# Kernel optimization log

Measured on AMD Instinct MI355X. Metric: run time of the kernel, lower is better.

The kernel has to match this reference:

```python
import jax, jax.numpy as jnp
import numpy as np

B, S, HID = 2, 2048, 1024
H, D = 16, 64  # num query heads, head_dim; single shared KV head
SCALE = D ** -0.5


def setup_inputs() -> dict:
    key = jax.random.key(0)
    k1, k2, k3, k4, k5 = jax.random.split(key, 5)
    return {
        "hidden_states": jax.random.normal(k1, (B, S, HID), dtype=jnp.float32),
        "Wq": jax.random.normal(k2, (HID, HID), dtype=jnp.float32) * 0.02,
        "Wk": jax.random.normal(k3, (HID, D), dtype=jnp.float32) * 0.02,
        "Wv": jax.random.normal(k4, (HID, D), dtype=jnp.float32) * 0.02,
        "Wo": jax.random.normal(k5, (HID, HID), dtype=jnp.float32) * 0.02,
    }


def reference(hidden_states, Wq, Wk, Wv, Wo):
    b, s, _ = hidden_states.shape
    # projections: Q has H heads; K/V have a single shared head of dim D
    q = (hidden_states @ Wq).reshape(b, s, H, D)  # [B,S,H,D]
    k = hidden_states @ Wk                        # [B,S,D]
    v = hidden_states @ Wv                        # [B,S,D]
    # scores: broadcast single KV head across all query heads
    scores = jnp.einsum("bqhd,bkd->bhqk", q, k) * SCALE  # [B,H,S,S]
    attn = jax.nn.softmax(scores, axis=-1)
    out = jnp.einsum("bhqk,bkd->bqhd", attn, v).reshape(b, s, HID)
    return out @ Wo
```

## Files before the change

kernel.cpp:

```cpp
#include <hip/hip_runtime.h>
#include <math.h>

#define BATCH 2
#define SEQ   2048
#define HID   1024
#define NH    16
#define HD    64
#define MTOT  (BATCH * SEQ)

#define PST 72
#define WTS 69

#define EXP_C1 0.1803368801111255f
#define EXP_C2 (-17.312340490667562f)

typedef __attribute__((ext_vector_type(8))) short short8;
typedef __attribute__((ext_vector_type(4))) float floatx4;
typedef __attribute__((ext_vector_type(16))) float floatx16;
typedef __attribute__((ext_vector_type(4))) unsigned int uint4v;

#define MFMA32(a, b, c) __builtin_amdgcn_mfma_f32_32x32x16_bf16(a, b, c, 0, 0, 0)

static __device__ __forceinline__ floatx16 zero16() {
    floatx16 z;
    #pragma unroll
    for (int i = 0; i < 16; ++i) z[i] = 0.f;
    return z;
}

__device__ __forceinline__ unsigned short f2bf(float x) {
    unsigned u = __float_as_uint(x);
    u += 0x7FFF + ((u >> 16) & 1);
    return (unsigned short)(u >> 16);
}
__device__ __forceinline__ float bf2f(unsigned short h) {
    return __uint_as_float((unsigned)h << 16);
}
__device__ __forceinline__ void split16(const float* f, unsigned short* hh, unsigned short* ll) {
    #pragma unroll
    for (int e = 0; e < 16; ++e) {
        unsigned short h = f2bf(f[e]);
        hh[e] = h;
        ll[e] = f2bf(f[e] - bf2f(h));
    }
}

__global__ __launch_bounds__(256)
void presplit_kernel(const float* __restrict__ Wq, const float* __restrict__ Wk,
                     const float* __restrict__ Wv, const float* __restrict__ Wo,
                     const float* __restrict__ X,
                     unsigned short* __restrict__ WqTh, unsigned short* __restrict__ WqTl,
                     unsigned short* __restrict__ WkTh, unsigned short* __restrict__ WkTl,
                     unsigned short* __restrict__ WvTh, unsigned short* __restrict__ WvTl,
                     unsigned short* __restrict__ WoTh, unsigned short* __restrict__ WoTl,
                     unsigned short* __restrict__ Xh)
{
    __shared__ __align__(16) float Wtmp[64][WTS];
    const int tid = threadIdx.x;
    int bx = blockIdx.x;

    if (bx >= 544) {
        size_t i0 = (size_t)(bx - 544) * 4096 + tid * 16;
        float f[16];
        *(float4*)&f[0]  = *(const float4*)(X + i0 + 0);
        *(float4*)&f[4]  = *(const float4*)(X + i0 + 4);
        *(float4*)&f[8]  = *(const float4*)(X + i0 + 8);
        *(float4*)&f[12] = *(const float4*)(X + i0 + 12);
        unsigned short hh[16];
        #pragma unroll
        for (int e = 0; e < 16; ++e) hh[e] = f2bf(f[e]);
        *(uint4*)(Xh + i0)     = *(uint4*)&hh[0];
        *(uint4*)(Xh + i0 + 8) = *(uint4*)&hh[8];
        return;
    }

    const float* W; unsigned short *Th, *Tl; int ldw, kt, nt;
    if (bx < 256)      { W = Wq; Th = WqTh; Tl = WqTl; ldw = HID; kt = bx >> 4; nt = bx & 15; }
    else if (bx < 272) { W = Wk; Th = WkTh; Tl = WkTl; ldw = HD;  kt = bx - 256; nt = 0; }
    else if (bx < 288) { W = Wv; Th = WvTh; Tl = WvTl; ldw = HD;  kt = bx - 272; nt = 0; }
    else               { W = Wo; Th = WoTh; Tl = WoTl; ldw = HID; bx -= 288; kt = bx >> 4; nt = bx & 15; }
    const int k0 = kt * 64, n0 = nt * 64;

    {
        const int wk = tid >> 2, wn = (tid & 3) * 16;
        const float* wp = W + (size_t)(k0 + wk) * ldw + n0 + wn;
        float f[16];
        *(float4*)&f[0]  = *(const float4*)(wp + 0);
        *(float4*)&f[4]  = *(const float4*)(wp + 4);
        *(float4*)&f[8]  = *(const float4*)(wp + 8);
        *(float4*)&f[12] = *(const float4*)(wp + 12);
        #pragma unroll
        for (int e = 0; e < 16; ++e) Wtmp[wk][wn + e] = f[e];
    }
    __syncthreads();
    {
        const int rn = tid >> 2, rk = (tid & 3) * 16;
        float f[16];
        #pragma unroll
        for (int e = 0; e < 16; ++e) f[e] = Wtmp[rk + e][rn];
        unsigned short hh[16], ll[16];
        split16(f, hh, ll);
        size_t off = (size_t)(n0 + rn) * HID + k0 + rk;
        *(uint4*)(Th + off)     = *(uint4*)&hh[0];
        *(uint4*)(Th + off + 8) = *(uint4*)&hh[8];
        *(uint4*)(Tl + off)     = *(uint4*)&ll[0];
        *(uint4*)(Tl + off + 8) = *(uint4*)&ll[8];
    }
}

__global__ __launch_bounds__(256)
void qkv_kernel(const unsigned short* __restrict__ Xh,
                const unsigned short* __restrict__ WqTh, const unsigned short* __restrict__ WqTl,
                const unsigned short* __restrict__ WkTh, const unsigned short* __restrict__ WkTl,
                const unsigned short* __restrict__ WvTh, const unsigned short* __restrict__ WvTl,
                unsigned short* __restrict__ Qh,
                unsigned short* __restrict__ Kh, unsigned short* __restrict__ Vth)
{
    __shared__ __align__(16) unsigned short Ah[128][PST];
    __shared__ __align__(16) unsigned short Wsh[64][PST], Wsl[64][PST];

    const int tid  = threadIdx.x;
    const int wave = tid >> 6, lane = tid & 63;
    const int t = lane & 15, quad = lane >> 4;
    const int m0 = blockIdx.x * 128;
    const int nb = blockIdx.y;

    const unsigned short *WTh, *WTl; int n0b;
    if (nb < 16)       { WTh = WqTh; WTl = WqTl; n0b = nb * 64; }
    else if (nb == 16) { WTh = WkTh; WTl = WkTl; n0b = 0; }
    else               { WTh = WvTh; WTl = WvTl; n0b = 0; }

    floatx4 acc[2][4];
    #pragma unroll
    for (int mi = 0; mi < 2; ++mi)
        #pragma unroll
        for (int sub = 0; sub < 4; ++sub) acc[mi][sub] = (floatx4){0.f,0.f,0.f,0.f};

    for (int kt = 0; kt < HID / 64; ++kt) {
        __syncthreads();
        #pragma unroll
        for (int i = 0; i < 4; ++i) {
            int c = tid + i * 256;
            int row = c >> 3, col8 = (c & 7) * 8;
            *(uint4*)&Ah[row][col8] =
                *(const uint4*)(Xh + (size_t)(m0 + row) * HID + kt * 64 + col8);
        }
        #pragma unroll
        for (int i = 0; i < 2; ++i) {
            int c = tid + i * 256;
            int row = c >> 3, col8 = (c & 7) * 8;
            size_t g = (size_t)(n0b + row) * HID + kt * 64 + col8;
            *(uint4*)&Wsh[row][col8] = *(const uint4*)(WTh + g);
            *(uint4*)&Wsl[row][col8] = *(const uint4*)(WTl + g);
        }
        __syncthreads();
        #pragma unroll
        for (int ks = 0; ks < 2; ++ks) {
            short8 bh[4], bl[4];
            #pragma unroll
            for (int sub = 0; sub < 4; ++sub) {
                bh[sub] = *(const short8*)&Wsh[sub * 16 + t][ks * 32 + quad * 8];
                bl[sub] = *(const short8*)&Wsl[sub * 16 + t][ks * 32 + quad * 8];
            }
            #pragma unroll
            for (int mi = 0; mi < 2; ++mi) {
                short8 ah = *(const short8*)&Ah[wave * 32 + mi * 16 + t][ks * 32 + quad * 8];
                #pragma unroll
                for (int sub = 0; sub < 4; ++sub) {
                    acc[mi][sub] = __builtin_amdgcn_mfma_f32_16x16x32_bf16(ah, bh[sub], acc[mi][sub], 0, 0, 0);
                    acc[mi][sub] = __builtin_amdgcn_mfma_f32_16x16x32_bf16(ah, bl[sub], acc[mi][sub], 0, 0, 0);
                }
            }
        }
    }

    #pragma unroll
    for (int mi = 0; mi < 2; ++mi)
        #pragma unroll
        for (int sub = 0; sub < 4; ++sub)
            #pragma unroll
            for (int r = 0; r < 4; ++r) {
                int g = m0 + wave * 32 + mi * 16 + quad * 4 + r;
                int d = sub * 16 + t;
                unsigned short hh = f2bf(acc[mi][sub][r]);
                if (nb < 16) {
                    int b = g >> 11, s = g & (SEQ - 1);
                    Qh[((size_t)(b * NH + nb) * SEQ + s) * HD + d] = hh;
                } else if (nb == 16) {
                    Kh[(size_t)g * HD + d] = hh;
                } else {
                    int b = g >> 11, s = g & (SEQ - 1);
                    Vth[(size_t)b * HD * SEQ + (size_t)d * SEQ + s] = hh;
                }
            }
}

__global__ __launch_bounds__(512, 4)
void flash_kernel(const unsigned short* __restrict__ Qhg,
                  const unsigned short* __restrict__ Khg,
                  const unsigned short* __restrict__ Vthg,
                  unsigned short* __restrict__ Oh)
{
    __shared__ __align__(16) char smem[33792];
    unsigned short (*Ksh)[PST] = (unsigned short (*)[PST])smem;
    unsigned short (*Vsh)[PST] = (unsigned short (*)[PST])(smem + 64 * PST * 2);

    const int tid  = threadIdx.x;
    const int wave = tid >> 6, lane = tid & 63;
    const int lq = lane & 31, hi = lane >> 5;
    const int qw = wave >> 1;
    const int ks = wave & 1;

    const int q0 = blockIdx.x * 128;
    const int h  = blockIdx.y;
    const int b  = blockIdx.z;

    short8 qreg[4];
    {
        const unsigned short* qp =
            Qhg + ((size_t)(b * NH + h) * SEQ + q0 + qw * 32 + lq) * HD + hi * 8;
        #pragma unroll
        for (int dc = 0; dc < 4; ++dc) qreg[dc] = *(const short8*)(qp + dc * 16);
    }

    const unsigned short* Kh_b  = Khg  + (size_t)b * SEQ * HD;
    const unsigned short* Vth_b = Vthg + (size_t)b * HD * SEQ;

    const int sr = tid >> 3, sc = (tid & 7) * 8;

    float l_part = 0.f;
    floatx16 o0 = zero16(), o1 = zero16();

    uint4 gk = *(const uint4*)(Kh_b + (size_t)sr * HD + sc);
    uint4 gv = *(const uint4*)(Vth_b + (size_t)sr * SEQ + sc);

    for (int kt = 0; kt < SEQ / 64; ++kt) {
        __syncthreads();
        *(uint4*)&Ksh[sr][sc] = gk;
        *(uint4*)&Vsh[sr][sc] = gv;
        if (kt + 1 < SEQ / 64) {
            gk = *(const uint4*)(Kh_b + (size_t)((kt + 1) * 64 + sr) * HD + sc);
            gv = *(const uint4*)(Vth_b + (size_t)sr * SEQ + (kt + 1) * 64 + sc);
        }
        __syncthreads();

        floatx16 sf = zero16();
        __builtin_amdgcn_s_setprio(1);
        #pragma unroll
        for (int dc = 0; dc < 4; ++dc) {
            short8 kf = *(const short8*)&Ksh[ks * 32 + lq][dc * 16 + hi * 8];
            sf = MFMA32(kf, qreg[dc], sf);
        }
        __builtin_amdgcn_s_setprio(0);

        unsigned w0[4], w1[4];
        #pragma unroll
        for (int rr = 0; rr < 4; ++rr) {
            unsigned u0 = __float_as_uint(exp2f(fmaf(sf[rr * 4 + 0], EXP_C1, EXP_C2)));
            unsigned u1 = __float_as_uint(exp2f(fmaf(sf[rr * 4 + 1], EXP_C1, EXP_C2)));
            unsigned u2 = __float_as_uint(exp2f(fmaf(sf[rr * 4 + 2], EXP_C1, EXP_C2)));
            unsigned u3 = __float_as_uint(exp2f(fmaf(sf[rr * 4 + 3], EXP_C1, EXP_C2)));
            l_part += __uint_as_float(u0 & 0xFFFF0000u) + __uint_as_float(u1 & 0xFFFF0000u)
                    + __uint_as_float(u2 & 0xFFFF0000u) + __uint_as_float(u3 & 0xFFFF0000u);
            w0[rr] = (u0 >> 16) | (u1 & 0xFFFF0000u);
            w1[rr] = (u2 >> 16) | (u3 & 0xFFFF0000u);
        }

        #pragma unroll
        for (int mm = 0; mm < 2; ++mm) {
            unsigned send0 = hi ? w0[2 * mm] : w0[2 * mm + 1];
            unsigned send1 = hi ? w1[2 * mm] : w1[2 * mm + 1];
            unsigned recv0 = (unsigned)__shfl_xor((int)send0, 32);
            unsigned recv1 = (unsigned)__shfl_xor((int)send1, 32);
            unsigned own0 = hi ? w0[2 * mm + 1] : w0[2 * mm];
            unsigned own1 = hi ? w1[2 * mm + 1] : w1[2 * mm];
            uint4v pw;
            pw.x = hi ? recv0 : own0;
            pw.y = hi ? recv1 : own1;
            pw.z = hi ? own0 : recv0;
            pw.w = hi ? own1 : recv1;
            short8 pa = __builtin_bit_cast(short8, pw);
            short8 v0 = *(const short8*)&Vsh[lq][ks * 32 + mm * 16 + hi * 8];
            short8 v1 = *(const short8*)&Vsh[32 + lq][ks * 32 + mm * 16 + hi * 8];
            __builtin_amdgcn_s_setprio(1);
            o0 = MFMA32(pa, v0, o0);
            o1 = MFMA32(pa, v1, o1);
            __builtin_amdgcn_s_setprio(0);
        }
    }

    float l_wave = l_part + __shfl_xor(l_part, 32);
    __syncthreads();
    float* cb = (float*)smem;
    const int cbase = (qw * 64 + lane) * 33;
    if (ks) {
        #pragma unroll
        for (int r = 0; r < 16; ++r) { cb[cbase + r] = o0[r]; cb[cbase + 16 + r] = o1[r]; }
        cb[cbase + 32] = l_wave;
    }
    __syncthreads();
    if (!ks) {
        float l_tot = l_wave + cb[cbase + 32];
        #pragma unroll
        for (int r = 0; r < 16; ++r) {
            int qr = (r & 3) + 8 * (r >> 2) + 4 * hi;
            float inv = 1.0f / __shfl(l_tot, qr);
            float a0 = o0[r] + cb[cbase + r];
            float a1 = o1[r] + cb[cbase + 16 + r];
            size_t row = (size_t)(b * SEQ + q0 + qw * 32 + qr) * HID + h * HD;
            Oh[row + lq]      = f2bf(a0 * inv);
            Oh[row + 32 + lq] = f2bf(a1 * inv);
        }
    }
}

__global__ __launch_bounds__(256)
void out_proj_kernel(const unsigned short* __restrict__ Ohg,
                     const unsigned short* __restrict__ WoTh,
                     const unsigned short* __restrict__ WoTl,
                     float* __restrict__ out)
{
    __shared__ __align__(16) unsigned short Ah[128][PST];
    __shared__ __align__(16) unsigned short Wsh[64][PST], Wsl[64][PST];

    const int tid  = threadIdx.x;
    const int wave = tid >> 6, lane = tid & 63;
    const int t = lane & 15, quad = lane >> 4;
    const int m0 = blockIdx.x * 128;
    const int n0 = blockIdx.y * 64;

    floatx4 acc[2][4];
    #pragma unroll
    for (int mi = 0; mi < 2; ++mi)
        #pragma unroll
        for (int sub = 0; sub < 4; ++sub) acc[mi][sub] = (floatx4){0.f,0.f,0.f,0.f};

    for (int kt = 0; kt < HID / 64; ++kt) {
        __syncthreads();
        #pragma unroll
        for (int i = 0; i < 4; ++i) {
            int c = tid + i * 256;
            int row = c >> 3, col8 = (c & 7) * 8;
            *(uint4*)&Ah[row][col8] =
                *(const uint4*)(Ohg + (size_t)(m0 + row) * HID + kt * 64 + col8);
        }
        #pragma unroll
        for (int i = 0; i < 2; ++i) {
            int c = tid + i * 256;
            int row = c >> 3, col8 = (c & 7) * 8;
            size_t g = (size_t)(n0 + row) * HID + kt * 64 + col8;
            *(uint4*)&Wsh[row][col8] = *(const uint4*)(WoTh + g);
            *(uint4*)&Wsl[row][col8] = *(const uint4*)(WoTl + g);
        }
        __syncthreads();
        #pragma unroll
        for (int ks = 0; ks < 2; ++ks) {
            short8 bh[4], bl[4];
            #pragma unroll
            for (int sub = 0; sub < 4; ++sub) {
                bh[sub] = *(const short8*)&Wsh[sub * 16 + t][ks * 32 + quad * 8];
                bl[sub] = *(const short8*)&Wsl[sub * 16 + t][ks * 32 + quad * 8];
            }
            #pragma unroll
            for (int mi = 0; mi < 2; ++mi) {
                short8 ah = *(const short8*)&Ah[wave * 32 + mi * 16 + t][ks * 32 + quad * 8];
                #pragma unroll
                for (int sub = 0; sub < 4; ++sub) {
                    acc[mi][sub] = __builtin_amdgcn_mfma_f32_16x16x32_bf16(ah, bh[sub], acc[mi][sub], 0, 0, 0);
                    acc[mi][sub] = __builtin_amdgcn_mfma_f32_16x16x32_bf16(ah, bl[sub], acc[mi][sub], 0, 0, 0);
                }
            }
        }
    }

    #pragma unroll
    for (int mi = 0; mi < 2; ++mi)
        #pragma unroll
        for (int sub = 0; sub < 4; ++sub)
            #pragma unroll
            for (int r = 0; r < 4; ++r)
                out[(size_t)(m0 + wave * 32 + mi * 16 + quad * 4 + r) * HID
                    + n0 + sub * 16 + t] = acc[mi][sub][r];
}

extern "C" void kernel_launch(void* const* d_in, const int* in_sizes, int n_in,
                              void* d_out, int out_size, void* d_ws, size_t ws_size,
                              hipStream_t stream)
{
    const float* X  = (const float*)d_in[0];
    const float* Wq = (const float*)d_in[1];
    const float* Wk = (const float*)d_in[2];
    const float* Wv = (const float*)d_in[3];
    const float* Wo = (const float*)d_in[4];
    float* out = (float*)d_out;

    unsigned short* Qh = (unsigned short*)d_out;
    unsigned short* Xh = Qh + (size_t)BATCH * NH * SEQ * HD;

    char* ws = (char*)d_ws;
    const size_t SZ_WQ = (size_t)HID * HID * 2;
    const size_t SZ_WK = (size_t)HD * HID * 2;
    unsigned short* WqTh = (unsigned short*)(ws);
    unsigned short* WqTl = (unsigned short*)(ws + SZ_WQ);
    unsigned short* WkTh = (unsigned short*)(ws + 2*SZ_WQ);
    unsigned short* WkTl = (unsigned short*)(ws + 2*SZ_WQ + SZ_WK);
    unsigned short* WvTh = (unsigned short*)(ws + 2*SZ_WQ + 2*SZ_WK);
    unsigned short* WvTl = (unsigned short*)(ws + 2*SZ_WQ + 3*SZ_WK);
    unsigned short* WoTh = (unsigned short*)(ws + 2*SZ_WQ + 4*SZ_WK);
    unsigned short* WoTl = (unsigned short*)(ws + 3*SZ_WQ + 4*SZ_WK);
    unsigned short* Kh   = (unsigned short*)(ws + 4*SZ_WQ + 4*SZ_WK);
    unsigned short* Vth  = (unsigned short*)(ws + 4*SZ_WQ + 4*SZ_WK + (size_t)MTOT*HD*2);
    unsigned short* Oh   = (unsigned short*)(ws + 4*SZ_WQ + 4*SZ_WK + (size_t)MTOT*HD*4);

    presplit_kernel<<<dim3(1568), 256, 0, stream>>>(Wq, Wk, Wv, Wo, X,
        WqTh, WqTl, WkTh, WkTl, WvTh, WvTl, WoTh, WoTl, Xh);
    qkv_kernel<<<dim3(MTOT / 128, 18), 256, 0, stream>>>(Xh,
        WqTh, WqTl, WkTh, WkTl, WvTh, WvTl, Qh, Kh, Vth);
    flash_kernel<<<dim3(SEQ / 128, NH, BATCH), 512, 0, stream>>>(Qh, Kh, Vth, Oh);
    out_proj_kernel<<<dim3(MTOT / 128, HID / 64), 256, 0, stream>>>(Oh, WoTh, WoTl, out);
}
```

Baseline: 199.4 us.

## Store GEMM operands in MFMA fragment order and load weights via global_load_lds

```diff
diff --git a/kernel.cpp b/kernel.cpp
--- a/kernel.cpp
+++ b/kernel.cpp
@@ -20,6 +20,7 @@
 typedef __attribute__((ext_vector_type(4))) unsigned int uint4v;
 
 #define MFMA32(a, b, c) __builtin_amdgcn_mfma_f32_32x32x16_bf16(a, b, c, 0, 0, 0)
+#define MFMA16(a, b, c) __builtin_amdgcn_mfma_f32_16x16x32_bf16(a, b, c, 0, 0, 0)
 
 static __device__ __forceinline__ floatx16 zero16() {
     floatx16 z;
@@ -44,6 +45,13 @@
         ll[e] = f2bf(f[e] - bf2f(h));
     }
 }
+
+__device__ __forceinline__ void gld16(const unsigned short* g, unsigned short* l) {
+    __builtin_amdgcn_global_load_lds(
+        (const __attribute__((address_space(1))) unsigned int*)g,
+        (__attribute__((address_space(3))) unsigned int*)l, 16, 0, 0);
+}
+
 
 __global__ __launch_bounds__(256)
 void presplit_kernel(const float* __restrict__ Wq, const float* __restrict__ Wk,
@@ -69,8 +77,17 @@
         unsigned short hh[16];
         #pragma unroll
         for (int e = 0; e < 16; ++e) hh[e] = f2bf(f[e]);
-        *(uint4*)(Xh + i0)     = *(uint4*)&hh[0];
-        *(uint4*)(Xh + i0 + 8) = *(uint4*)&hh[8];
+        const int m  = (bx - 544) * 4 + (tid >> 6);
+        const int k0 = (tid & 63) * 16;
+        const int m32 = m >> 5, mi = (m >> 4) & 1, tr = m & 15;
+        #pragma unroll
+        for (int c = 0; c < 2; ++c) {
+            const int k = k0 + c * 8;
+            const int ktx = k >> 6, ksx = (k >> 5) & 1, qd = (k >> 3) & 3;
+            size_t off = (((size_t)(m32 * 16 + ktx) * 2 + ksx) * 2 + mi) * 512
+                       + (qd * 16 + tr) * 8;
+            *(uint4*)(Xh + off) = *(uint4*)&hh[c * 8];
+        }
         return;
     }
 
@@ -100,24 +117,28 @@
         for (int e = 0; e < 16; ++e) f[e] = Wtmp[rk + e][rn];
         unsigned short hh[16], ll[16];
         split16(f, hh, ll);
-        size_t off = (size_t)(n0 + rn) * HID + k0 + rk;
-        *(uint4*)(Th + off)     = *(uint4*)&hh[0];
-        *(uint4*)(Th + off + 8) = *(uint4*)&hh[8];
-        *(uint4*)(Tl + off)     = *(uint4*)&ll[0];
-        *(uint4*)(Tl + off + 8) = *(uint4*)&ll[8];
+        const int sub = rn >> 4, tw = rn & 15;
+        const size_t tb = ((size_t)nt * 16 + kt) * 4096;
+        const int ksA = rk >> 5,       qA = (rk >> 3) & 3;
+        const int ksB = (rk + 8) >> 5, qB = ((rk + 8) >> 3) & 3;
+        const size_t offA = tb + (size_t)(ksA * 4 + sub) * 512 + (qA * 16 + tw) * 8;
+        const size_t offB = tb + (size_t)(ksB * 4 + sub) * 512 + (qB * 16 + tw) * 8;
+        *(uint4*)(Th + offA) = *(uint4*)&hh[0];
+        *(uint4*)(Th + offB) = *(uint4*)&hh[8];
+        *(uint4*)(Tl + offA) = *(uint4*)&ll[0];
+        *(uint4*)(Tl + offB) = *(uint4*)&ll[8];
     }
 }
 
 __global__ __launch_bounds__(256)
-void qkv_kernel(const unsigned short* __restrict__ Xh,
+void qkv_kernel(const unsigned short* __restrict__ Xfo,
                 const unsigned short* __restrict__ WqTh, const unsigned short* __restrict__ WqTl,
                 const unsigned short* __restrict__ WkTh, const unsigned short* __restrict__ WkTl,
                 const unsigned short* __restrict__ WvTh, const unsigned short* __restrict__ WvTl,
                 unsigned short* __restrict__ Qh,
                 unsigned short* __restrict__ Kh, unsigned short* __restrict__ Vth)
 {
-    __shared__ __align__(16) unsigned short Ah[128][PST];
-    __shared__ __align__(16) unsigned short Wsh[64][PST], Wsl[64][PST];
+    __shared__ __align__(16) unsigned short Wst[2][4096];
 
     const int tid  = threadIdx.x;
     const int wave = tid >> 6, lane = tid & 63;
@@ -125,10 +146,10 @@
     const int m0 = blockIdx.x * 128;
     const int nb = blockIdx.y;
 
-    const unsigned short *WTh, *WTl; int n0b;
-    if (nb < 16)       { WTh = WqTh; WTl = WqTl; n0b = nb * 64; }
-    else if (nb == 16) { WTh = WkTh; WTl = WkTl; n0b = 0; }
-    else               { WTh = WvTh; WTl = WvTl; n0b = 0; }
+    const unsigned short *WTh, *WTl; int nt;
+    if (nb < 16)       { WTh = WqTh; WTl = WqTl; nt = nb; }
+    else if (nb == 16) { WTh = WkTh; WTl = WkTl; nt = 0; }
+    else               { WTh = WvTh; WTl = WvTl; nt = 0; }
 
     floatx4 acc[2][4];
     #pragma unroll
@@ -136,40 +157,39 @@
         #pragma unroll
         for (int sub = 0; sub < 4; ++sub) acc[mi][sub] = (floatx4){0.f,0.f,0.f,0.f};
 
+    const size_t abase = ((size_t)(blockIdx.x * 4 + wave) * 16) * 2048 + lane * 8;
+    const int g0 = wave * 2;
+
     for (int kt = 0; kt < HID / 64; ++kt) {
         __syncthreads();
-        #pragma unroll
-        for (int i = 0; i < 4; ++i) {
-            int c = tid + i * 256;
-            int row = c >> 3, col8 = (c & 7) * 8;
-            *(uint4*)&Ah[row][col8] =
-                *(const uint4*)(Xh + (size_t)(m0 + row) * HID + kt * 64 + col8);
-        }
-        #pragma unroll
-        for (int i = 0; i < 2; ++i) {
-            int c = tid + i * 256;
-            int row = c >> 3, col8 = (c & 7) * 8;
-            size_t g = (size_t)(n0b + row) * HID + kt * 64 + col8;
-            *(uint4*)&Wsh[row][col8] = *(const uint4*)(WTh + g);
-            *(uint4*)&Wsl[row][col8] = *(const uint4*)(WTl + g);
-        }
-        __syncthreads();
-        #pragma unroll
-        for (int ks = 0; ks < 2; ++ks) {
-            short8 bh[4], bl[4];
+        {
+            const size_t tb = ((size_t)nt * 16 + kt) * 4096 + g0 * 512 + lane * 8;
+            gld16(WTh + tb,       &Wst[0][g0 * 512]);
+            gld16(WTh + tb + 512, &Wst[0][g0 * 512 + 512]);
+            gld16(WTl + tb,       &Wst[1][g0 * 512]);
+            gld16(WTl + tb + 512, &Wst[1][g0 * 512 + 512]);
+        }
+        __syncthreads();
+
+        const unsigned short* ab = Xfo + abase + (size_t)kt * 2048;
+        short8 a00 = *(const short8*)(ab);
+        short8 a01 = *(const short8*)(ab + 512);
+        short8 a10 = *(const short8*)(ab + 1024);
+        short8 a11 = *(const short8*)(ab + 1536);
+
+        #pragma unroll
+        for (int ksq = 0; ksq < 2; ++ksq) {
+            short8 am0 = ksq ? a10 : a00;
+            short8 am1 = ksq ? a11 : a01;
             #pragma unroll
             for (int sub = 0; sub < 4; ++sub) {
-                bh[sub] = *(const short8*)&Wsh[sub * 16 + t][ks * 32 + quad * 8];
-                bl[sub] = *(const short8*)&Wsl[sub * 16 + t][ks * 32 + quad * 8];
-            }
-            #pragma unroll
-            for (int mi = 0; mi < 2; ++mi) {
-                short8 ah = *(const short8*)&Ah[wave * 32 + mi * 16 + t][ks * 32 + quad * 8];
-                #pragma unroll
-                for (int sub = 0; sub < 4; ++sub) {
-                    acc[mi][sub] = __builtin_amdgcn_mfma_f32_16x16x32_bf16(ah, bh[sub], acc[mi][sub], 0, 0, 0);
-                    acc[mi][sub] = __builtin_amdgcn_mfma_f32_16x16x32_bf16(ah, bl[sub], acc[mi][sub], 0, 0, 0);
-                }
+                const int g = ksq * 4 + sub;
+                short8 bh = *(const short8*)&Wst[0][g * 512 + lane * 8];
+                short8 bl = *(const short8*)&Wst[1][g * 512 + lane * 8];
+                acc[0][sub] = MFMA16(am0, bh, acc[0][sub]);
+                acc[0][sub] = MFMA16(am0, bl, acc[0][sub]);
+                acc[1][sub] = MFMA16(am1, bh, acc[1][sub]);
+                acc[1][sub] = MFMA16(am1, bl, acc[1][sub]);
             }
         }
     }
@@ -301,33 +321,35 @@
     __syncthreads();
     if (!ks) {
         float l_tot = l_wave + cb[cbase + 32];
+        const int m32 = b * 64 + blockIdx.x * 4 + qw;
         #pragma unroll
         for (int r = 0; r < 16; ++r) {
             int qr = (r & 3) + 8 * (r >> 2) + 4 * hi;
             float inv = 1.0f / __shfl(l_tot, qr);
             float a0 = o0[r] + cb[cbase + r];
             float a1 = o1[r] + cb[cbase + 16 + r];
-            size_t row = (size_t)(b * SEQ + q0 + qw * 32 + qr) * HID + h * HD;
-            Oh[row + lq]      = f2bf(a0 * inv);
-            Oh[row + 32 + lq] = f2bf(a1 * inv);
+            int mi = qr >> 4, tr = qr & 15;
+            size_t base = (((size_t)(m32 * 16 + h) * 2 + 0) * 2 + mi) * 512
+                        + ((lq >> 3) * 16 + tr) * 8 + (lq & 7);
+            Oh[base]        = f2bf(a0 * inv);
+            Oh[base + 1024] = f2bf(a1 * inv);
         }
     }
 }
 
 __global__ __launch_bounds__(256)
-void out_proj_kernel(const unsigned short* __restrict__ Ohg,
+void out_proj_kernel(const unsigned short* __restrict__ Ofo,
                      const unsigned short* __restrict__ WoTh,
                      const unsigned short* __restrict__ WoTl,
                      float* __restrict__ out)
 {
-    __shared__ __align__(16) unsigned short Ah[128][PST];
-    __shared__ __align__(16) unsigned short Wsh[64][PST], Wsl[64][PST];
+    __shared__ __align__(16) unsigned short Wst[2][4096];
 
     const int tid  = threadIdx.x;
     const int wave = tid >> 6, lane = tid & 63;
     const int t = lane & 15, quad = lane >> 4;
     const int m0 = blockIdx.x * 128;
-    const int n0 = blockIdx.y * 64;
+    const int nt = blockIdx.y;
 
     floatx4 acc[2][4];
     #pragma unroll
@@ -335,44 +357,44 @@
         #pragma unroll
         for (int sub = 0; sub < 4; ++sub) acc[mi][sub] = (floatx4){0.f,0.f,0.f,0.f};
 
+    const size_t abase = ((size_t)(blockIdx.x * 4 + wave) * 16) * 2048 + lane * 8;
+    const int g0 = wave * 2;
+
     for (int kt = 0; kt < HID / 64; ++kt) {
         __syncthreads();
-        #pragma unroll
-        for (int i = 0; i < 4; ++i) {
-            int c = tid + i * 256;
-            int row = c >> 3, col8 = (c & 7) * 8;
-            *(uint4*)&Ah[row][col8] =
-                *(const uint4*)(Ohg + (size_t)(m0 + row) * HID + kt * 64 + col8);
-        }
-        #pragma unroll
-        for (int i = 0; i < 2; ++i) {
-            int c = tid + i * 256;
-            int row = c >> 3, col8 = (c & 7) * 8;
-            size_t g = (size_t)(n0 + row) * HID + kt * 64 + col8;
-            *(uint4*)&Wsh[row][col8] = *(const uint4*)(WoTh + g);
-            *(uint4*)&Wsl[row][col8] = *(const uint4*)(WoTl + g);
-        }
-        __syncthreads();
-        #pragma unroll
-        for (int ks = 0; ks < 2; ++ks) {
-            short8 bh[4], bl[4];
+        {
+            const size_t tb = ((size_t)nt * 16 + kt) * 4096 + g0 * 512 + lane * 8;
+            gld16(WoTh + tb,       &Wst[0][g0 * 512]);
+            gld16(WoTh + tb + 512, &Wst[0][g0 * 512 + 512]);
+            gld16(WoTl + tb,       &Wst[1][g0 * 512]);
+            gld16(WoTl + tb + 512, &Wst[1][g0 * 512 + 512]);
+        }
+        __syncthreads();
+
+        const unsigned short* ab = Ofo + abase + (size_t)kt * 2048;
+        short8 a00 = *(const short8*)(ab);
+        short8 a01 = *(const short8*)(ab + 512);
+        short8 a10 = *(const short8*)(ab + 1024);
+        short8 a11 = *(const short8*)(ab + 1536);
+
+        #pragma unroll
+        for (int ksq = 0; ksq < 2; ++ksq) {
+            short8 am0 = ksq ? a10 : a00;
+            short8 am1 = ksq ? a11 : a01;
             #pragma unroll
             for (int sub = 0; sub < 4; ++sub) {
-                bh[sub] = *(const short8*)&Wsh[sub * 16 + t][ks * 32 + quad * 8];
-                bl[sub] = *(const short8*)&Wsl[sub * 16 + t][ks * 32 + quad * 8];
+                const int g = ksq * 4 + sub;
+                short8 bh = *(const short8*)&Wst[0][g * 512 + lane * 8];
+                short8 bl = *(const short8*)&Wst[1][g * 512 + lane * 8];
+                acc[0][sub] = MFMA16(am0, bh, acc[0][sub]);
+                acc[0][sub] = MFMA16(am0, bl, acc[0][sub]);
+                acc[1][sub] = MFMA16(am1, bh, acc[1][sub]);
+                acc[1][sub] = MFMA16(am1, bl, acc[1][sub]);
             }
-            #pragma unroll
-            for (int mi = 0; mi < 2; ++mi) {
-                short8 ah = *(const short8*)&Ah[wave * 32 + mi * 16 + t][ks * 32 + quad * 8];
-                #pragma unroll
-                for (int sub = 0; sub < 4; ++sub) {
-                    acc[mi][sub] = __builtin_amdgcn_mfma_f32_16x16x32_bf16(ah, bh[sub], acc[mi][sub], 0, 0, 0);
-                    acc[mi][sub] = __builtin_amdgcn_mfma_f32_16x16x32_bf16(ah, bl[sub], acc[mi][sub], 0, 0, 0);
-                }
-            }
-        }
-    }
-
+        }
+    }
+
+    const int n0 = nt * 64;
     #pragma unroll
     for (int mi = 0; mi < 2; ++mi)
         #pragma unroll
```

Measured after the change: 189.3 us. 1.05x faster.
